# Optimization experiments

Hardware: AMD Instinct MI355X
Metric: run time of the kernel (lower is better)

The kernel has to match this reference:

```python
import jax, jax.numpy as jnp
import numpy as np

V, E, L, ENC, P, B = 10000, 512, 30, 2048, 196, 64
A = E  # attention_dim == embedding_dim


def _lin(key, out_d, in_d, scale=0.02):
    kW, kb = jax.random.split(key)
    return (jax.random.normal(kW, (out_d, in_d), jnp.float32) * scale,
            jax.random.normal(kb, (out_d,), jnp.float32) * scale)


def setup_inputs() -> dict:
    key = jax.random.key(0)
    ks = jax.random.split(key, 12)
    enc_out = jax.random.normal(ks[0], (B, P, ENC), jnp.float32)
    dec_in = jax.random.randint(ks[1], (B, L), 0, V, jnp.int64)
    emb = jax.random.normal(ks[2], (V, E), jnp.float32) * 0.02
    We, be = _lin(ks[3], A, ENC)      # attention.encoder_att
    Wd, bd = _lin(ks[4], A, E)        # attention.decoder_att
    Wf, bf = _lin(ks[5], 1, A)        # attention.full_att
    Wih, bih = _lin(ks[6], 4 * E, E + ENC)  # lstm weight_ih_l0 (i,f,g,o)
    Whh, bhh = _lin(ks[7], 4 * E, E)        # lstm weight_hh_l0
    Wh0, bh0 = _lin(ks[8], E, ENC)    # init_h
    Wc0, bc0 = _lin(ks[9], E, ENC)    # init_c
    Wv, bv = _lin(ks[10], V, E)       # emb2voca
    return dict(enc_out=enc_out, dec_in=dec_in, epoch=1, emb=emb,
                We=We, be=be, Wd=Wd, bd=bd, Wf=Wf, bf=bf,
                Wih=Wih, bih=bih, Whh=Whh, bhh=bhh,
                Wh0=Wh0, bh0=bh0, Wc0=Wc0, bc0=bc0, Wv=Wv, bv=bv)


def reference(enc_out, dec_in, epoch, emb, We, be, Wd, bd, Wf, bf,
              Wih, bih, Whh, bhh, Wh0, bh0, Wc0, bc0, Wv, bv):
    max_len = dec_in.shape[1]
    mean = enc_out.mean(axis=1)                     # [B, ENC]
    h = mean @ Wh0.T + bh0                          # [B, E]
    c = mean @ Wc0.T + bc0                          # [B, E]
    emb_in = emb[dec_in]                            # [B, L, E]
    inp0 = emb_in[:, 0]                             # [B, E]
    att1 = enc_out @ We.T + be                      # [B, P, A] (hidden-independent)

    def step(carry, _):
        h, c, inp = carry
        att2 = h @ Wd.T + bd                        # [B, A]
        score = jax.nn.relu(att1 + att2[:, None, :])  # [B, P, A]
        e = jnp.squeeze(score @ Wf.T + bf, -1)      # [B, P]
        att = jax.nn.softmax(e, axis=1)
        ctx = jnp.einsum('bp,bpd->bd', att, enc_out)  # [B, ENC]
        x = jnp.concatenate([ctx, inp], axis=1)     # [B, ENC+E]
        gates = x @ Wih.T + bih + h @ Whh.T + bhh   # [B, 4E]
        i, f, g, o = jnp.split(gates, 4, axis=1)
        c_new = jax.nn.sigmoid(f) * c + jax.nn.sigmoid(i) * jnp.tanh(g)
        h_new = jax.nn.sigmoid(o) * jnp.tanh(c_new)
        logits = h_new @ Wv.T + bv                  # [B, V]
        inp_new = emb[jnp.argmax(logits, axis=-1)]  # greedy feedback (eval path)
        return (h_new, c_new, inp_new), (logits, att)

    _, (logits, atts) = jax.lax.scan(step, (h, c, inp0), None, length=max_len)
    return logits.transpose(1, 0, 2), atts.transpose(1, 0, 2)  # [B,L,V], [B,L,P]
```

## Files before the change

kernel.cpp:

```cpp
#include <hip/hip_runtime.h>
#include <math.h>

constexpr int B_   = 64;
constexpr int L_   = 30;
constexpr int P_   = 196;
constexpr int ENC_ = 2048;
constexpr int V_   = 10000;
constexpr int XSTR = 3072;
constexpr unsigned NB = 256;
constexpr int SUBCH = 512;

__device__ __forceinline__ float sigmf(float x) { return 1.0f / (1.0f + expf(-x)); }

__device__ __forceinline__ float dot16(const float4* w, const float* xp) {
    const float4* x4 = (const float4*)xp;
    float4 x0 = x4[0], x1 = x4[1], x2 = x4[2], x3 = x4[3];
    float s = w[0].x * x0.x;
    s = fmaf(w[0].y, x0.y, s); s = fmaf(w[0].z, x0.z, s); s = fmaf(w[0].w, x0.w, s);
    s = fmaf(w[1].x, x1.x, s); s = fmaf(w[1].y, x1.y, s);
    s = fmaf(w[1].z, x1.z, s); s = fmaf(w[1].w, x1.w, s);
    s = fmaf(w[2].x, x2.x, s); s = fmaf(w[2].y, x2.y, s);
    s = fmaf(w[2].z, x2.z, s); s = fmaf(w[2].w, x2.w, s);
    s = fmaf(w[3].x, x3.x, s); s = fmaf(w[3].y, x3.y, s);
    s = fmaf(w[3].z, x3.z, s); s = fmaf(w[3].w, x3.w, s);
    return s;
}

__device__ __forceinline__ float2 cload2(const float* p) {
    unsigned long long v = __hip_atomic_load((const unsigned long long*)p,
                                             __ATOMIC_RELAXED, __HIP_MEMORY_SCOPE_AGENT);
    union { unsigned long long u; float2 f; } c; c.u = v; return c.f;
}
__device__ __forceinline__ void cstore2(float* p, float2 v) {
    union { float2 f; unsigned long long u; } c; c.f = v;
    __hip_atomic_store((unsigned long long*)p, c.u,
                       __ATOMIC_RELAXED, __HIP_MEMORY_SCOPE_AGENT);
}
__device__ __forceinline__ float cload(const float* p) {
    unsigned v = __hip_atomic_load((const unsigned*)p,
                                   __ATOMIC_RELAXED, __HIP_MEMORY_SCOPE_AGENT);
    return __uint_as_float(v);
}
__device__ __forceinline__ void cstore(float* p, float v) {
    __hip_atomic_store((unsigned*)p, __float_as_uint(v),
                       __ATOMIC_RELAXED, __HIP_MEMORY_SCOPE_AGENT);
}
__device__ __forceinline__ float4 ntload4(const float* p) {
    typedef float v4f __attribute__((ext_vector_type(4)));
    v4f t = __builtin_nontemporal_load((const v4f*)p);
    return make_float4(t.x, t.y, t.z, t.w);
}

__device__ __forceinline__ void gbar(unsigned* flags, unsigned* gen, unsigned seq) {
    asm volatile("s_waitcnt vmcnt(0)" ::: "memory");
    __syncthreads();
    if (blockIdx.x == 0) {
        int i = threadIdx.x;
        if (i >= 1 && i < (int)NB) {
            while (__hip_atomic_load(&flags[i], __ATOMIC_RELAXED,
                                     __HIP_MEMORY_SCOPE_AGENT) < seq)
                __builtin_amdgcn_s_sleep(4);
        }
        __syncthreads();
        if (i == 0)
            __hip_atomic_store(gen, seq, __ATOMIC_RELAXED, __HIP_MEMORY_SCOPE_AGENT);
    } else {
        if (threadIdx.x == 0) {
            __hip_atomic_store(&flags[blockIdx.x], seq,
                               __ATOMIC_RELAXED, __HIP_MEMORY_SCOPE_AGENT);
            while (__hip_atomic_load(gen, __ATOMIC_RELAXED,
                                     __HIP_MEMORY_SCOPE_AGENT) < seq)
                __builtin_amdgcn_s_sleep(4);
        }
        __syncthreads();
    }
    asm volatile("" ::: "memory");
}

__global__ __launch_bounds__(256) void k_init(const float* __restrict__ enc,
                                              float* __restrict__ mean,
                                              unsigned* __restrict__ bar) {
    if (blockIdx.x == 0 && blockIdx.y == 0) {
        bar[threadIdx.x] = 0u;
        if (threadIdx.x == 0) bar[256] = 0u;
    }
    int dc = blockIdx.x, b = blockIdx.y, d = dc * 256 + threadIdx.x;
    const float* base = enc + (size_t)b * P_ * ENC_ + d;
    float s = 0.f;
    for (int p = 0; p < P_; p++) s += base[(size_t)p * ENC_];
    mean[(size_t)b * ENC_ + d] = s / 196.0f;
}

__global__ __launch_bounds__(256) void k_big(
    const float* __restrict__ enc, const float* __restrict__ mean,
    const float* __restrict__ We, const float* __restrict__ be,
    const float* __restrict__ Wh0, const float* __restrict__ bh0,
    const float* __restrict__ Wc0, const float* __restrict__ bc0,
    float* __restrict__ att1, float* __restrict__ X, float* __restrict__ cbuf) {
    __shared__ __align__(16) float As[16][132];
    __shared__ __align__(16) float Ws[16][132];
    int gx = blockIdx.x;
    const float *A, *W, *bias;
    float* C;
    int m0, n0, Mtot, cstr;
    if (gx < 392) {
        A = enc; W = We; bias = be; C = att1;
        m0 = (gx >> 2) * 128; n0 = (gx & 3) * 128; Mtot = 12544; cstr = 512;
    } else if (gx < 396) {
        A = mean; W = Wh0; bias = bh0; C = X + 2560;
        m0 = 0; n0 = (gx - 392) * 128; Mtot = 64; cstr = XSTR;
    } else {
        A = mean; W = Wc0; bias = bc0; C = cbuf;
        m0 = 0; n0 = (gx - 396) * 128; Mtot = 64; cstr = 512;
    }
    int tid = threadIdx.x, tx = tid & 15, ty = tid >> 4;
    int srow = tid >> 2, skq = tid & 3;
    float acc[2][2][4][4] = {};
    int r0 = m0 + min(srow, Mtot - 1);
    int r1 = m0 + min(srow + 64, Mtot - 1);
    const float* a0p = A + (size_t)r0 * 2048 + skq * 4;
    const float* a1p = A + (size_t)r1 * 2048 + skq * 4;
    const float* w0p = W + (size_t)(n0 + srow) * 2048 + skq * 4;
    const float* w1p = W + (size_t)(n0 + srow + 64) * 2048 + skq * 4;
    for (int kk = 0; kk < 2048; kk += 16) {
        float4 a0v = *(const float4*)(a0p + kk);
        float4 a1v = *(const float4*)(a1p + kk);
        float4 w0v = *(const float4*)(w0p + kk);
        float4 w1v = *(const float4*)(w1p + kk);
        __syncthreads();
        As[skq * 4 + 0][srow] = a0v.x; As[skq * 4 + 1][srow] = a0v.y;
        As[skq * 4 + 2][srow] = a0v.z; As[skq * 4 + 3][srow] = a0v.w;
        As[skq * 4 + 0][srow + 64] = a1v.x; As[skq * 4 + 1][srow + 64] = a1v.y;
        As[skq * 4 + 2][srow + 64] = a1v.z; As[skq * 4 + 3][srow + 64] = a1v.w;
        Ws[skq * 4 + 0][srow] = w0v.x; Ws[skq * 4 + 1][srow] = w0v.y;
        Ws[skq * 4 + 2][srow] = w0v.z; Ws[skq * 4 + 3][srow] = w0v.w;
        Ws[skq * 4 + 0][srow + 64] = w1v.x; Ws[skq * 4 + 1][srow + 64] = w1v.y;
        Ws[skq * 4 + 2][srow + 64] = w1v.z; Ws[skq * 4 + 3][srow + 64] = w1v.w;
        __syncthreads();
#pragma unroll
        for (int k = 0; k < 16; k++) {
            float4 av0 = *(const float4*)&As[k][ty * 4];
            float4 av1 = *(const float4*)&As[k][64 + ty * 4];
            float4 bv0 = *(const float4*)&Ws[k][tx * 4];
            float4 bv1 = *(const float4*)&Ws[k][64 + tx * 4];
            float ar[2][4] = {{av0.x, av0.y, av0.z, av0.w}, {av1.x, av1.y, av1.z, av1.w}};
            float br[2][4] = {{bv0.x, bv0.y, bv0.z, bv0.w}, {bv1.x, bv1.y, bv1.z, bv1.w}};
#pragma unroll
            for (int ih = 0; ih < 2; ih++)
#pragma unroll
                for (int jh = 0; jh < 2; jh++)
#pragma unroll
                    for (int i = 0; i < 4; i++)
#pragma unroll
                        for (int j = 0; j < 4; j++)
                            acc[ih][jh][i][j] = fmaf(ar[ih][i], br[jh][j], acc[ih][jh][i][j]);
        }
    }
#pragma unroll
    for (int ih = 0; ih < 2; ih++)
#pragma unroll
        for (int i = 0; i < 4; i++) {
            int m = m0 + ih * 64 + ty * 4 + i;
            if (m - m0 < Mtot) {
#pragma unroll
                for (int jh = 0; jh < 2; jh++) {
                    int n = n0 + jh * 64 + tx * 4;
                    float4 o;
                    o.x = acc[ih][jh][i][0] + bias[n + 0];
                    o.y = acc[ih][jh][i][1] + bias[n + 1];
                    o.z = acc[ih][jh][i][2] + bias[n + 2];
                    o.w = acc[ih][jh][i][3] + bias[n + 3];
                    *(float4*)(C + (size_t)m * cstr + n) = o;
                }
            }
        }
}

__global__ __launch_bounds__(256) void k_emb0(const float* __restrict__ emb,
                                              const int* __restrict__ dec,
                                              float* __restrict__ X) {
    int b = blockIdx.x, tid = threadIdx.x;
    int tok = dec[b * L_];
    X[(size_t)b * XSTR + 2048 + tid] = emb[(size_t)tok * 512 + tid];
    X[(size_t)b * XSTR + 2048 + 256 + tid] = emb[(size_t)tok * 512 + 256 + tid];
}


__device__ __forceinline__ void ph_gates(int bid, int tid, int wid, int lane,
                                         const float* X, const float* Wih,
                                         const float* Whh, float* pg,
                                         int kcT, int chunk, float* s_stage) {
    bool act = (bid < 8 * kcT);
    int nthigh = bid & 3;
    int kc = (bid >> 2) & (kcT - 1);
    int bh = act ? ((bid >> 2) / kcT) : 0;
    int nt = nthigh * 8 + wid;
    int row = nt * 64 + lane;
    const float* wih_row = Wih + (size_t)row * 2560;
    const float* whh_row = Whh + (size_t)row * 512;
    int kbase = kc * chunk;
    float acc[32];
#pragma unroll
    for (int b = 0; b < 32; b++) acc[b] = 0.f;
    for (int sc = 0; sc < chunk; sc += SUBCH) {
        int cl = min(SUBCH, chunk - sc);
        if (act) {
            int hcl = cl >> 1;
            for (int bb = wid * 4; bb < wid * 4 + 4; bb++) {
                const float* xr = X + (size_t)(bh * 32 + bb) * XSTR + kbase + sc;
                float* sr = s_stage + bb * SUBCH;
                for (int j2 = lane; j2 < hcl; j2 += 64)
                    *(float2*)&sr[j2 * 2] = cload2(xr + j2 * 2);
            }
        }
        __syncthreads();
        if (act) {
#pragma unroll 1
            for (int k16 = sc; k16 < sc + cl; k16 += 16) {
                int kk = kbase + k16;
                const float* wr = (kk < 2560) ? (wih_row + kk) : (whh_row + (kk - 2560));
                float4 w[4];
                w[0] = *(const float4*)(wr);
                w[1] = *(const float4*)(wr + 4);
                w[2] = *(const float4*)(wr + 8);
                w[3] = *(const float4*)(wr + 12);
                const float* xc = s_stage + (k16 - sc);
#pragma unroll
                for (int b = 0; b < 32; b++)
                    acc[b] += dot16(w, xc + b * SUBCH);
            }
        }
        __syncthreads();
    }
    if (act) {
        float* prow = pg + ((size_t)kc * 64 + bh * 32) * 2048 + row;
#pragma unroll
        for (int b = 0; b < 32; b++)
            cstore(prow + (size_t)b * 2048, acc[b]);
    }
}

__device__ __forceinline__ void ph_lstm(int bid, int tid, const float* pg,
                                        const float* bih, const float* bhh,
                                        float* X, float* cbuf, int kcT,
                                        float* s_g) {
    if (bid >= 128) return;
    int b = bid >> 1, jh = bid & 1;
    int jl = tid & 255, gi2 = tid >> 8;
    int j = jh * 256 + jl;
#pragma unroll
    for (int gg = 0; gg < 2; gg++) {
        int gi = gi2 * 2 + gg;
        int n = gi * 512 + j;
        float s = bih[n] + bhh[n];
#pragma unroll 4
        for (int kc = 0; kc < kcT; kc++)
            s += cload(pg + ((size_t)kc * 64 + b) * 2048 + n);
        s_g[gi * 256 + jl] = s;
    }
    __syncthreads();
    if (gi2 == 0) {
        float gi_ = s_g[0 * 256 + jl], gf = s_g[1 * 256 + jl];
        float gc = s_g[2 * 256 + jl], go = s_g[3 * 256 + jl];
        float c = cbuf[b * 512 + j];
        float cn = sigmf(gf) * c + sigmf(gi_) * tanhf(gc);
        float hn = sigmf(go) * tanhf(cn);
        cbuf[b * 512 + j] = cn;
        cstore(X + (size_t)b * XSTR + 2560 + j, hn);
    }
}

__device__ __forceinline__ void ph_hstage(bool act, int wid, int lane,
                                          const float* X, float* s_stage) {
    if (act) {
        for (int b = wid * 8; b < wid * 8 + 8; b++) {
            const float* xr = X + (size_t)b * XSTR + 2560;
            float* sr = s_stage + b * 512;
            for (int j2 = lane; j2 < 256; j2 += 64)
                *(float2*)&sr[j2 * 2] = cload2(xr + j2 * 2);
        }
    }
    __syncthreads();
}

__device__ __forceinline__ void ph_logits(int bid, int wid, int lane,
                                          const float* s_stage, const float* Wv,
                                          const float* bv, float* out,
                                          float* pargmax, int t) {
    int v = bid * 64 + lane;
    int vr = min(v, V_ - 1);
    const float* wrow = Wv + (size_t)vr * 512;
    const float* xbase = s_stage + wid * 8 * 512;
    float acc[8];
#pragma unroll
    for (int b = 0; b < 8; b++) acc[b] = 0.f;
#pragma unroll 1
    for (int k16 = 0; k16 < 512; k16 += 16) {
        float4 w[4];
        w[0] = *(const float4*)(wrow + k16);
        w[1] = *(const float4*)(wrow + k16 + 4);
        w[2] = *(const float4*)(wrow + k16 + 8);
        w[3] = *(const float4*)(wrow + k16 + 12);
        const float* xc = xbase + k16;
#pragma unroll
        for (int b = 0; b < 8; b++)
            acc[b] += dot16(w, xc + b * 512);
    }
    float bias = bv[vr];
#pragma unroll
    for (int b = 0; b < 8; b++) {
        float val = acc[b] + bias;
        int bb = wid * 8 + b;
        if (v < V_) out[((size_t)bb * L_ + t) * V_ + v] = val;
        float mval = (v < V_) ? val : -INFINITY;
        int midx = v;
#pragma unroll
        for (int m = 32; m >= 1; m >>= 1) {
            float ov = __shfl_xor(mval, m, 64);
            int oi = __shfl_xor(midx, m, 64);
            if (ov > mval || (ov == mval && oi < midx)) { mval = ov; midx = oi; }
        }
        if (lane == 0)
            cstore2(pargmax + ((size_t)bb * 157 + bid) * 2,
                    make_float2(mval, (float)midx));
    }
}

__device__ __forceinline__ void ph_att2c(int bid, int wid, int lane,
                                         const float* s_stage, const float* Wd,
                                         const float* bd, float* att2buf) {
    int task = (bid - 157) * 8 + wid;
    int nt = task >> 3, bg = task & 7;
    int n = nt * 64 + lane;
    const float* wrow = Wd + (size_t)n * 512;
    const float* xbase = s_stage + bg * 8 * 512;
    float acc[8];
#pragma unroll
    for (int b = 0; b < 8; b++) acc[b] = 0.f;
#pragma unroll 1
    for (int k16 = 0; k16 < 512; k16 += 16) {
        float4 w[4];
        w[0] = *(const float4*)(wrow + k16);
        w[1] = *(const float4*)(wrow + k16 + 4);
        w[2] = *(const float4*)(wrow + k16 + 8);
        w[3] = *(const float4*)(wrow + k16 + 12);
        const float* xc = xbase + k16;
#pragma unroll
        for (int b = 0; b < 8; b++)
            acc[b] += dot16(w, xc + b * 512);
    }
    float bias = bd[n];
#pragma unroll
    for (int b = 0; b < 8; b++)
        cstore(att2buf + (size_t)(bg * 8 + b) * 512 + n, acc[b] + bias);
}

__device__ __forceinline__ void ph_e(int bid, int tid, int wid, int lane,
                                     const float* att1, const float* att2buf,
                                     const float* Wf, const float* bfp,
                                     float* attbuf, float* atts_out, int t,
                                     float* s_att2, float* s_e, float* s_red) {
    int b = bid;
    if (tid < 256)
        *(float2*)&s_att2[tid * 2] = cload2(att2buf + (size_t)b * 512 + tid * 2);
    __syncthreads();
    const float4* a24 = (const float4*)s_att2;
    float4 t0 = a24[lane], t1 = a24[lane + 64];
    const float4* wf4 = (const float4*)Wf;
    float4 f0 = wf4[lane], f1 = wf4[lane + 64];
    float bfv = bfp[0];
    for (int p = wid; p < P_; p += 8) {
        const float4* rr = (const float4*)(att1 + ((size_t)b * P_ + p) * 512);
        float4 v0 = rr[lane], v1 = rr[lane + 64];
        float s = fmaxf(v0.x + t0.x, 0.f) * f0.x + fmaxf(v0.y + t0.y, 0.f) * f0.y +
                  fmaxf(v0.z + t0.z, 0.f) * f0.z + fmaxf(v0.w + t0.w, 0.f) * f0.w +
                  fmaxf(v1.x + t1.x, 0.f) * f1.x + fmaxf(v1.y + t1.y, 0.f) * f1.y +
                  fmaxf(v1.z + t1.z, 0.f) * f1.z + fmaxf(v1.w + t1.w, 0.f) * f1.w;
#pragma unroll
        for (int m = 32; m >= 1; m >>= 1) s += __shfl_xor(s, m, 64);
        if (lane == 0) s_e[p] = s + bfv;
    }
    __syncthreads();
    float val = -INFINITY;
    if (tid < 256) {
        val = (tid < P_) ? s_e[tid] : -INFINITY;
        s_red[tid] = val;
    }
    __syncthreads();
    for (int s = 128; s > 0; s >>= 1) {
        if (tid < s) s_red[tid] = fmaxf(s_red[tid], s_red[tid + s]);
        __syncthreads();
    }
    float m = s_red[0];
    __syncthreads();
    float ex = (tid < P_) ? expf(val - m) : 0.f;
    if (tid < 256) s_red[tid] = ex;
    __syncthreads();
    for (int s = 128; s > 0; s >>= 1) {
        if (tid < s) s_red[tid] += s_red[tid + s];
        __syncthreads();
    }
    float sum = s_red[0];
    if (tid < P_) {
        float att = ex / sum;
        cstore(attbuf + b * 256 + tid, att);
        atts_out[((size_t)b * L_ + t) * P_ + tid] = att;
    }
}

__device__ __forceinline__ void ph_fin(int bid, int wid, int lane,
                                       const float* pargmax, const float* emb,
                                       float* X) {
    int b = (bid - 200) * 8 + wid;
    float best = -INFINITY;
    int bi = V_;
    for (int i = lane; i < 157; i += 64) {
        float2 pm = cload2(pargmax + ((size_t)b * 157 + i) * 2);
        int idx = (int)pm.y;
        if (pm.x > best || (pm.x == best && idx < bi)) { best = pm.x; bi = idx; }
    }
#pragma unroll
    for (int m = 32; m >= 1; m >>= 1) {
        float ob = __shfl_xor(best, m, 64);
        int oi = __shfl_xor(bi, m, 64);
        if (ob > best || (ob == best && oi < bi)) { best = ob; bi = oi; }
    }
    const float4* e4 = (const float4*)(emb + (size_t)bi * 512);
    float4 v0 = e4[lane], v1 = e4[lane + 64];
    float* xp = X + (size_t)b * XSTR + 2048;
    cstore2(xp + lane * 4,           make_float2(v0.x, v0.y));
    cstore2(xp + lane * 4 + 2,       make_float2(v0.z, v0.w));
    cstore2(xp + 256 + lane * 4,     make_float2(v1.x, v1.y));
    cstore2(xp + 256 + lane * 4 + 2, make_float2(v1.z, v1.w));
}

__device__ __forceinline__ void ph_ctx2(int bid, int tid, const float* enc,
                                        const float* attbuf, float* X,
                                        float* s_att, float* s_stage) {
    int b = bid >> 2, dq = bid & 3;
    if (tid < P_) s_att[tid] = cload(attbuf + b * 256 + tid);
    __syncthreads();
    int dl = tid & 127, pg4 = tid >> 7;
    int d = dq * 512 + dl * 4;
    const float* base = enc + (size_t)b * P_ * ENC_ + d;
    float4 acc = make_float4(0.f, 0.f, 0.f, 0.f);
#pragma unroll 7
    for (int p = pg4; p < P_; p += 4) {
        float w = s_att[p];
        float4 v = ntload4(base + (size_t)p * ENC_);
        acc.x = fmaf(w, v.x, acc.x);
        acc.y = fmaf(w, v.y, acc.y);
        acc.z = fmaf(w, v.z, acc.z);
        acc.w = fmaf(w, v.w, acc.w);
    }
    float4* sc4 = (float4*)s_stage;
    sc4[pg4 * 128 + dl] = acc;
    __syncthreads();
    if (tid < 128) {
        float4 r0 = sc4[tid], r1 = sc4[128 + tid];
        float4 r2 = sc4[256 + tid], r3 = sc4[384 + tid];
        float4 o;
        o.x = (r0.x + r1.x) + (r2.x + r3.x);
        o.y = (r0.y + r1.y) + (r2.y + r3.y);
        o.z = (r0.z + r1.z) + (r2.z + r3.z);
        o.w = (r0.w + r1.w) + (r2.w + r3.w);
        float* xp = X + (size_t)b * XSTR + dq * 512 + tid * 4;
        cstore2(xp,     make_float2(o.x, o.y));
        cstore2(xp + 2, make_float2(o.z, o.w));
    }
    __syncthreads();
}

__global__ __launch_bounds__(512, 2) void k_mega(
    const float* __restrict__ enc, const float* __restrict__ emb,
    const float* __restrict__ Wd, const float* __restrict__ bd,
    const float* __restrict__ Wf, const float* __restrict__ bfp,
    const float* __restrict__ Wih, const float* __restrict__ bih,
    const float* __restrict__ Whh, const float* __restrict__ bhh,
    const float* __restrict__ Wv, const float* __restrict__ bv,
    const float* __restrict__ att1, float* __restrict__ X,
    float* __restrict__ cbuf, float* __restrict__ att2buf,
    float* __restrict__ attbuf, float* __restrict__ pargmax,
    float* __restrict__ pg, float* __restrict__ out,
    float* __restrict__ atts_out, unsigned* __restrict__ bar,
    int kcT, int chunk) {
    const int bid = blockIdx.x, tid = threadIdx.x;
    const int wid = tid >> 6, lane = tid & 63;
    __shared__ __align__(16) float s_stage[64 * SUBCH];
    __shared__ __align__(16) float s_att2[512];
    __shared__ float s_e[256];
    __shared__ float s_red[256];
    __shared__ float s_att[256];
    __shared__ float s_g[4 * 256];
    unsigned* flags = bar;
    unsigned* gen = bar + 256;
    unsigned seq = 1;

    ph_hstage(bid >= 157 && bid < 165, wid, lane, X, s_stage);
    if (bid >= 157 && bid < 165) ph_att2c(bid, wid, lane, s_stage, Wd, bd, att2buf);
    gbar(flags, gen, seq); seq++;
    if (bid < 64)
        ph_e(bid, tid, wid, lane, att1, att2buf, Wf, bfp, attbuf, atts_out, 0,
             s_att2, s_e, s_red);
    gbar(flags, gen, seq); seq++;
    ph_ctx2(bid, tid, enc, attbuf, X, s_att, s_stage);
    gbar(flags, gen, seq); seq++;

#pragma unroll 1
    for (int t = 0; t < L_; ++t) {
        ph_gates(bid, tid, wid, lane, X, Wih, Whh, pg, kcT, chunk, s_stage);
        gbar(flags, gen, seq); seq++;
        ph_lstm(bid, tid, pg, bih, bhh, X, cbuf, kcT, s_g);
        gbar(flags, gen, seq); seq++;
        ph_hstage(bid < 165, wid, lane, X, s_stage);
        if (bid < 157) ph_logits(bid, wid, lane, s_stage, Wv, bv, out, pargmax, t);
        else if (bid < 165 && t < L_ - 1)
            ph_att2c(bid, wid, lane, s_stage, Wd, bd, att2buf);
        if (t == L_ - 1) break;
        gbar(flags, gen, seq); seq++;
        if (bid < 64)
            ph_e(bid, tid, wid, lane, att1, att2buf, Wf, bfp, attbuf, atts_out,
                 t + 1, s_att2, s_e, s_red);
        else if (bid >= 200 && bid < 208)
            ph_fin(bid, wid, lane, pargmax, emb, X);
        gbar(flags, gen, seq); seq++;
        ph_ctx2(bid, tid, enc, attbuf, X, s_att, s_stage);
        gbar(flags, gen, seq); seq++;
    }
}

extern "C" void kernel_launch(void* const* d_in, const int* in_sizes, int n_in,
                              void* d_out, int out_size, void* d_ws, size_t ws_size,
                              hipStream_t stream) {
    const float* enc = (const float*)d_in[0];
    const int* dec   = (const int*)d_in[1];
    const float* emb = (const float*)d_in[3];
    const float* We  = (const float*)d_in[4];
    const float* be  = (const float*)d_in[5];
    const float* Wd  = (const float*)d_in[6];
    const float* bd  = (const float*)d_in[7];
    const float* Wf  = (const float*)d_in[8];
    const float* bf  = (const float*)d_in[9];
    const float* Wih = (const float*)d_in[10];
    const float* bih = (const float*)d_in[11];
    const float* Whh = (const float*)d_in[12];
    const float* bhh = (const float*)d_in[13];
    const float* Wh0 = (const float*)d_in[14];
    const float* bh0 = (const float*)d_in[15];
    const float* Wc0 = (const float*)d_in[16];
    const float* bc0 = (const float*)d_in[17];
    const float* Wv  = (const float*)d_in[18];
    const float* bv  = (const float*)d_in[19];

    float* out = (float*)d_out;
    float* ws = (float*)d_ws;

    float* att1    = ws;
    float* X       = att1 + 6422528;
    float* cbuf    = X + 196608;
    float* att2buf = cbuf + 32768;
    float* attbuf  = att2buf + 32768;
    float* pargmax = attbuf + 16384;
    unsigned* bar  = (unsigned*)(pargmax + 20480);
    float* pg      = ws + 6722048;
    float* mean    = pg;

    const size_t base_fl = 6722048;
    size_t avail_fl = ws_size / 4;
    int kcT = 2, chunk = 1536;
    const int opt_kc[5] = {32, 16, 8, 4, 2};
    for (int i = 0; i < 5; i++) {
        if (avail_fl >= base_fl + (size_t)opt_kc[i] * 131072) {
            kcT = opt_kc[i];
            chunk = 3072 / kcT;
            break;
        }
    }

    float* atts_out = out + (size_t)B_ * L_ * V_;

    hipLaunchKernelGGL(k_init, dim3(8, 64), dim3(256), 0, stream, enc, mean, bar);
    hipLaunchKernelGGL(k_big, dim3(400), dim3(256), 0, stream, enc, mean, We, be,
                       Wh0, bh0, Wc0, bc0, att1, X, cbuf);
    hipLaunchKernelGGL(k_emb0, dim3(64), dim3(256), 0, stream, emb, dec, X);
    hipLaunchKernelGGL(k_mega, dim3(NB), dim3(512), 0, stream,
                       enc, emb, Wd, bd, Wf, bf, Wih, bih, Whh, bhh, Wv, bv,
                       att1, X, cbuf, att2buf, attbuf, pargmax, pg, out,
                       atts_out, bar, kcT, chunk);
}
```

Before: 4.293 ms.

## Double persistent megakernel block to 1024 threads and remap all phases

The persistent recurrent kernel now launches 1024 threads per block instead of 512, and every phase is remapped onto 16 waves. The gates GEMM tiles 16 batches per block with a single staging pass instead of sub-chunks. The LSTM, logits, att2, ctx and argmax-finish phases are re-partitioned to match, and the minimum K-split is raised to 8. The aim is more latency hiding and parallelism in each grid-barrier-separated phase, at the cost of higher register and LDS pressure per block and a changed reduction order. The ctx loads also switch from nontemporal to normal loads.

```diff
diff --git a/kernel.cpp b/kernel.cpp
--- a/kernel.cpp
+++ b/kernel.cpp
@@ -8,7 +8,6 @@
 constexpr int V_   = 10000;
 constexpr int XSTR = 3072;
 constexpr unsigned NB = 256;
-constexpr int SUBCH = 512;
 
 __device__ __forceinline__ float sigmf(float x) { return 1.0f / (1.0f + expf(-x)); }
 
@@ -44,11 +43,6 @@
 __device__ __forceinline__ void cstore(float* p, float v) {
     __hip_atomic_store((unsigned*)p, __float_as_uint(v),
                        __ATOMIC_RELAXED, __HIP_MEMORY_SCOPE_AGENT);
-}
-__device__ __forceinline__ float4 ntload4(const float* p) {
-    typedef float v4f __attribute__((ext_vector_type(4)));
-    v4f t = __builtin_nontemporal_load((const v4f*)p);
-    return make_float4(t.x, t.y, t.z, t.w);
 }
 
 __device__ __forceinline__ void gbar(unsigned* flags, unsigned* gen, unsigned seq) {
@@ -191,51 +185,40 @@
                                          const float* Whh, float* pg,
                                          int kcT, int chunk, float* s_stage) {
     bool act = (bid < 8 * kcT);
-    int nthigh = bid & 3;
-    int kc = (bid >> 2) & (kcT - 1);
-    int bh = act ? ((bid >> 2) / kcT) : 0;
-    int nt = nthigh * 8 + wid;
+    int rowT = bid / (kcT * 4);
+    int kc = (bid >> 2) % kcT;
+    int bh = bid & 3;
+    int nt = rowT * 16 + wid;
     int row = nt * 64 + lane;
     const float* wih_row = Wih + (size_t)row * 2560;
     const float* whh_row = Whh + (size_t)row * 512;
     int kbase = kc * chunk;
-    float acc[32];
-#pragma unroll
-    for (int b = 0; b < 32; b++) acc[b] = 0.f;
-    for (int sc = 0; sc < chunk; sc += SUBCH) {
-        int cl = min(SUBCH, chunk - sc);
-        if (act) {
-            int hcl = cl >> 1;
-            for (int bb = wid * 4; bb < wid * 4 + 4; bb++) {
-                const float* xr = X + (size_t)(bh * 32 + bb) * XSTR + kbase + sc;
-                float* sr = s_stage + bb * SUBCH;
-                for (int j2 = lane; j2 < hcl; j2 += 64)
-                    *(float2*)&sr[j2 * 2] = cload2(xr + j2 * 2);
-            }
-        }
-        __syncthreads();
-        if (act) {
+    if (act && wid < 16) {
+        const float* xr = X + (size_t)(bh * 16 + wid) * XSTR + kbase;
+        float* sr = s_stage + wid * chunk;
+        for (int j = lane; j < chunk; j += 64) sr[j] = cload(xr + j);
+    }
+    __syncthreads();
+    if (act) {
+        float acc[16];
+#pragma unroll
+        for (int b = 0; b < 16; b++) acc[b] = 0.f;
 #pragma unroll 1
-            for (int k16 = sc; k16 < sc + cl; k16 += 16) {
-                int kk = kbase + k16;
-                const float* wr = (kk < 2560) ? (wih_row + kk) : (whh_row + (kk - 2560));
-                float4 w[4];
-                w[0] = *(const float4*)(wr);
-                w[1] = *(const float4*)(wr + 4);
-                w[2] = *(const float4*)(wr + 8);
-                w[3] = *(const float4*)(wr + 12);
-                const float* xc = s_stage + (k16 - sc);
-#pragma unroll
-                for (int b = 0; b < 32; b++)
-                    acc[b] += dot16(w, xc + b * SUBCH);
-            }
-        }
-        __syncthreads();
-    }
-    if (act) {
-        float* prow = pg + ((size_t)kc * 64 + bh * 32) * 2048 + row;
-#pragma unroll
-        for (int b = 0; b < 32; b++)
+        for (int k16 = 0; k16 < chunk; k16 += 16) {
+            int kk = kbase + k16;
+            const float* wr = (kk < 2560) ? (wih_row + kk) : (whh_row + (kk - 2560));
+            float4 w[4];
+            w[0] = *(const float4*)(wr);
+            w[1] = *(const float4*)(wr + 4);
+            w[2] = *(const float4*)(wr + 8);
+            w[3] = *(const float4*)(wr + 12);
+#pragma unroll
+            for (int b = 0; b < 16; b++)
+                acc[b] += dot16(w, s_stage + b * chunk + k16);
+        }
+        float* prow = pg + ((size_t)kc * 64 + bh * 16) * 2048 + row;
+#pragma unroll
+        for (int b = 0; b < 16; b++)
             cstore(prow + (size_t)b * 2048, acc[b]);
     }
 }
@@ -244,24 +227,21 @@
                                         const float* bih, const float* bhh,
                                         float* X, float* cbuf, int kcT,
                                         float* s_g) {
-    if (bid >= 128) return;
-    int b = bid >> 1, jh = bid & 1;
-    int jl = tid & 255, gi2 = tid >> 8;
-    int j = jh * 256 + jl;
-#pragma unroll
-    for (int gg = 0; gg < 2; gg++) {
-        int gi = gi2 * 2 + gg;
-        int n = gi * 512 + j;
+    int b = bid >> 2, jq = bid & 3;
+    if (tid < 512) {
+        int gi = tid >> 7, jl = tid & 127;
+        int n = gi * 512 + jq * 128 + jl;
         float s = bih[n] + bhh[n];
-#pragma unroll 4
+#pragma unroll 8
         for (int kc = 0; kc < kcT; kc++)
             s += cload(pg + ((size_t)kc * 64 + b) * 2048 + n);
-        s_g[gi * 256 + jl] = s;
-    }
-    __syncthreads();
-    if (gi2 == 0) {
-        float gi_ = s_g[0 * 256 + jl], gf = s_g[1 * 256 + jl];
-        float gc = s_g[2 * 256 + jl], go = s_g[3 * 256 + jl];
+        s_g[gi * 128 + jl] = s;
+    }
+    __syncthreads();
+    if (tid < 128) {
+        int j = jq * 128 + tid;
+        float gi_ = s_g[tid], gf = s_g[128 + tid];
+        float gc = s_g[256 + tid], go = s_g[384 + tid];
         float c = cbuf[b * 512 + j];
         float cn = sigmf(gf) * c + sigmf(gi_) * tanhf(gc);
         float hn = sigmf(go) * tanhf(cn);
@@ -273,7 +253,7 @@
 __device__ __forceinline__ void ph_hstage(bool act, int wid, int lane,
                                           const float* X, float* s_stage) {
     if (act) {
-        for (int b = wid * 8; b < wid * 8 + 8; b++) {
+        for (int b = wid * 4; b < wid * 4 + 4; b++) {
             const float* xr = X + (size_t)b * XSTR + 2560;
             float* sr = s_stage + b * 512;
             for (int j2 = lane; j2 < 256; j2 += 64)
@@ -290,10 +270,10 @@
     int v = bid * 64 + lane;
     int vr = min(v, V_ - 1);
     const float* wrow = Wv + (size_t)vr * 512;
-    const float* xbase = s_stage + wid * 8 * 512;
-    float acc[8];
-#pragma unroll
-    for (int b = 0; b < 8; b++) acc[b] = 0.f;
+    const float* xbase = s_stage + wid * 4 * 512;
+    float acc[4];
+#pragma unroll
+    for (int b = 0; b < 4; b++) acc[b] = 0.f;
 #pragma unroll 1
     for (int k16 = 0; k16 < 512; k16 += 16) {
         float4 w[4];
@@ -303,14 +283,14 @@
         w[3] = *(const float4*)(wrow + k16 + 12);
         const float* xc = xbase + k16;
 #pragma unroll
-        for (int b = 0; b < 8; b++)
+        for (int b = 0; b < 4; b++)
             acc[b] += dot16(w, xc + b * 512);
     }
     float bias = bv[vr];
 #pragma unroll
-    for (int b = 0; b < 8; b++) {
+    for (int b = 0; b < 4; b++) {
         float val = acc[b] + bias;
-        int bb = wid * 8 + b;
+        int bb = wid * 4 + b;
         if (v < V_) out[((size_t)bb * L_ + t) * V_ + v] = val;
         float mval = (v < V_) ? val : -INFINITY;
         int midx = v;
@@ -329,14 +309,14 @@
 __device__ __forceinline__ void ph_att2c(int bid, int wid, int lane,
                                          const float* s_stage, const float* Wd,
                                          const float* bd, float* att2buf) {
-    int task = (bid - 157) * 8 + wid;
-    int nt = task >> 3, bg = task & 7;
+    int task = (bid - 157) * 16 + wid;
+    int nt = task >> 4, bq = task & 15;
     int n = nt * 64 + lane;
     const float* wrow = Wd + (size_t)n * 512;
-    const float* xbase = s_stage + bg * 8 * 512;
-    float acc[8];
-#pragma unroll
-    for (int b = 0; b < 8; b++) acc[b] = 0.f;
+    const float* xbase = s_stage + bq * 4 * 512;
+    float acc[4];
+#pragma unroll
+    for (int b = 0; b < 4; b++) acc[b] = 0.f;
 #pragma unroll 1
     for (int k16 = 0; k16 < 512; k16 += 16) {
         float4 w[4];
@@ -346,13 +326,13 @@
         w[3] = *(const float4*)(wrow + k16 + 12);
         const float* xc = xbase + k16;
 #pragma unroll
-        for (int b = 0; b < 8; b++)
+        for (int b = 0; b < 4; b++)
             acc[b] += dot16(w, xc + b * 512);
     }
     float bias = bd[n];
 #pragma unroll
-    for (int b = 0; b < 8; b++)
-        cstore(att2buf + (size_t)(bg * 8 + b) * 512 + n, acc[b] + bias);
+    for (int b = 0; b < 4; b++)
+        cstore(att2buf + (size_t)(bq * 4 + b) * 512 + n, acc[b] + bias);
 }
 
 __device__ __forceinline__ void ph_e(int bid, int tid, int wid, int lane,
@@ -369,7 +349,7 @@
     const float4* wf4 = (const float4*)Wf;
     float4 f0 = wf4[lane], f1 = wf4[lane + 64];
     float bfv = bfp[0];
-    for (int p = wid; p < P_; p += 8) {
+    for (int p = wid; p < P_; p += 16) {
         const float4* rr = (const float4*)(att1 + ((size_t)b * P_ + p) * 512);
         float4 v0 = rr[lane], v1 = rr[lane + 64];
         float s = fmaxf(v0.x + t0.x, 0.f) * f0.x + fmaxf(v0.y + t0.y, 0.f) * f0.y +
@@ -411,7 +391,7 @@
 __device__ __forceinline__ void ph_fin(int bid, int wid, int lane,
                                        const float* pargmax, const float* emb,
                                        float* X) {
-    int b = (bid - 200) * 8 + wid;
+    int b = (bid - 200) * 16 + wid;
     float best = -INFINITY;
     int bi = V_;
     for (int i = lane; i < 157; i += 64) {
@@ -440,38 +420,39 @@
     int b = bid >> 2, dq = bid & 3;
     if (tid < P_) s_att[tid] = cload(attbuf + b * 256 + tid);
     __syncthreads();
-    int dl = tid & 127, pg4 = tid >> 7;
+    int dl = tid & 127, pgr = tid >> 7;
     int d = dq * 512 + dl * 4;
     const float* base = enc + (size_t)b * P_ * ENC_ + d;
     float4 acc = make_float4(0.f, 0.f, 0.f, 0.f);
-#pragma unroll 7
-    for (int p = pg4; p < P_; p += 4) {
+#pragma unroll 4
+    for (int p = pgr; p < P_; p += 8) {
         float w = s_att[p];
-        float4 v = ntload4(base + (size_t)p * ENC_);
+        float4 v = *(const float4*)(base + (size_t)p * ENC_);
         acc.x = fmaf(w, v.x, acc.x);
         acc.y = fmaf(w, v.y, acc.y);
         acc.z = fmaf(w, v.z, acc.z);
         acc.w = fmaf(w, v.w, acc.w);
     }
     float4* sc4 = (float4*)s_stage;
-    sc4[pg4 * 128 + dl] = acc;
+    sc4[pgr * 128 + dl] = acc;
     __syncthreads();
     if (tid < 128) {
-        float4 r0 = sc4[tid], r1 = sc4[128 + tid];
+        float4 r0 = sc4[tid],       r1 = sc4[128 + tid];
         float4 r2 = sc4[256 + tid], r3 = sc4[384 + tid];
+        float4 r4 = sc4[512 + tid], r5 = sc4[640 + tid];
+        float4 r6 = sc4[768 + tid], r7 = sc4[896 + tid];
         float4 o;
-        o.x = (r0.x + r1.x) + (r2.x + r3.x);
-        o.y = (r0.y + r1.y) + (r2.y + r3.y);
-        o.z = (r0.z + r1.z) + (r2.z + r3.z);
-        o.w = (r0.w + r1.w) + (r2.w + r3.w);
+        o.x = ((r0.x + r1.x) + (r2.x + r3.x)) + ((r4.x + r5.x) + (r6.x + r7.x));
+        o.y = ((r0.y + r1.y) + (r2.y + r3.y)) + ((r4.y + r5.y) + (r6.y + r7.y));
+        o.z = ((r0.z + r1.z) + (r2.z + r3.z)) + ((r4.z + r5.z) + (r6.z + r7.z));
+        o.w = ((r0.w + r1.w) + (r2.w + r3.w)) + ((r4.w + r5.w) + (r6.w + r7.w));
         float* xp = X + (size_t)b * XSTR + dq * 512 + tid * 4;
         cstore2(xp,     make_float2(o.x, o.y));
         cstore2(xp + 2, make_float2(o.z, o.w));
     }
-    __syncthreads();
-}
-
-__global__ __launch_bounds__(512, 2) void k_mega(
+}
+
+__global__ __launch_bounds__(1024, 4) void k_mega(
     const float* __restrict__ enc, const float* __restrict__ emb,
     const float* __restrict__ Wd, const float* __restrict__ bd,
     const float* __restrict__ Wf, const float* __restrict__ bfp,
@@ -486,12 +467,12 @@
     int kcT, int chunk) {
     const int bid = blockIdx.x, tid = threadIdx.x;
     const int wid = tid >> 6, lane = tid & 63;
-    __shared__ __align__(16) float s_stage[64 * SUBCH];
+    __shared__ __align__(16) float s_stage[64 * 512];
     __shared__ __align__(16) float s_att2[512];
     __shared__ float s_e[256];
     __shared__ float s_red[256];
     __shared__ float s_att[256];
-    __shared__ float s_g[4 * 256];
+    __shared__ float s_g[512];
     unsigned* flags = bar;
     unsigned* gen = bar + 256;
     unsigned seq = 1;
@@ -521,7 +502,7 @@
         if (bid < 64)
             ph_e(bid, tid, wid, lane, att1, att2buf, Wf, bfp, attbuf, atts_out,
                  t + 1, s_att2, s_e, s_red);
-        else if (bid >= 200 && bid < 208)
+        else if (bid >= 200 && bid < 204)
             ph_fin(bid, wid, lane, pargmax, emb, X);
         gbar(flags, gen, seq); seq++;
         ph_ctx2(bid, tid, enc, attbuf, X, s_att, s_stage);
@@ -567,9 +548,9 @@
 
     const size_t base_fl = 6722048;
     size_t avail_fl = ws_size / 4;
-    int kcT = 2, chunk = 1536;
-    const int opt_kc[5] = {32, 16, 8, 4, 2};
-    for (int i = 0; i < 5; i++) {
+    int kcT = 8, chunk = 384;
+    const int opt_kc[3] = {32, 16, 8};
+    for (int i = 0; i < 3; i++) {
         if (avail_fl >= base_fl + (size_t)opt_kc[i] * 131072) {
             kcT = opt_kc[i];
             chunk = 3072 / kcT;
@@ -583,7 +564,7 @@
     hipLaunchKernelGGL(k_big, dim3(400), dim3(256), 0, stream, enc, mean, We, be,
                        Wh0, bh0, Wc0, bc0, att1, X, cbuf);
     hipLaunchKernelGGL(k_emb0, dim3(64), dim3(256), 0, stream, emb, dec, X);
-    hipLaunchKernelGGL(k_mega, dim3(NB), dim3(512), 0, stream,
+    hipLaunchKernelGGL(k_mega, dim3(NB), dim3(1024), 0, stream,
                        enc, emb, Wd, bd, Wf, bf, Wih, bih, Whh, bhh, Wv, bv,
                        att1, X, cbuf, att2buf, attbuf, pargmax, pg, out,
                        atts_out, bar, kcT, chunk);
```

Measured after the change: 5.165 ms. +20.3%, slower.
